# Optimization experiments

Hardware: AMD Instinct MI355X
Metric: run time of the kernel (lower is better)

The kernel has to match this reference:

```python
import jax, jax.numpy as jnp
import numpy as np

N = 2708       # hardcoded in the original forward (Cora)
INS = 1433
OUTS = 64
M = 8          # N_mechs
HID = 64       # conditioner hidden width
LEAK = 0.2
NEG = -1e9


def setup_inputs() -> dict:
    key = jax.random.key(0)
    ks = jax.random.split(key, 9)
    x = jax.random.normal(ks[0], (N, INS), dtype=jnp.float32)
    adj = jax.random.randint(ks[1], (N, N), 0, 2) > 0  # bool mask
    adj = adj | jnp.eye(N, dtype=bool)                 # ensure self-loops so softmax is well-defined
    s = 1.0 / np.sqrt(INS)
    W = jax.random.normal(ks[2], (M, INS, OUTS), dtype=jnp.float32) * s
    a_src = jax.random.normal(ks[3], (M, OUTS), dtype=jnp.float32) * (1.0 / np.sqrt(OUTS))
    a_dst = jax.random.normal(ks[4], (M, OUTS), dtype=jnp.float32) * (1.0 / np.sqrt(OUTS))
    Wc1 = jax.random.normal(ks[5], (INS, HID), dtype=jnp.float32) * s
    bc1 = jnp.zeros((HID,), dtype=jnp.float32)
    Wc2 = jax.random.normal(ks[6], (HID, 2 * M), dtype=jnp.float32) * (1.0 / np.sqrt(HID))
    bc2 = jnp.zeros((2 * M,), dtype=jnp.float32)
    return {"x": x, "adj": adj, "W": W, "a_src": a_src, "a_dst": a_dst,
            "Wc1": Wc1, "bc1": bc1, "Wc2": Wc2, "bc2": bc2}


def reference(x, adj, W, a_src, a_dst, Wc1, bc1, Wc2, bc2):
    # dropout is identity in eval mode.
    # Conditioner MLP applied per node (vectorized over the Python loop in the original):
    cond = jax.nn.relu(x @ Wc1 + bc1) @ Wc2 + bc2          # [N, 2M]
    c = cond.reshape(N, 2, M)                               # matches cond.view(2708, 2, -1)
    gamma = c[:, 0, :].T                                    # [M, N] per-node scalar gamma per mechanism
    beta = c[:, 1, :].T                                     # [M, N]
    # All mechanisms batched: project + FiLM modulate
    h = jnp.einsum('nf,mfo->mno', x, W)                     # [M, N, OUTS]
    h = gamma[:, :, None] * h + beta[:, :, None]
    # GAT scoring: e_ij = LeakyReLU(a_src.h_i + a_dst.h_j), masked by adj
    e_src = jnp.einsum('mno,mo->mn', h, a_src)              # [M, N]
    e_dst = jnp.einsum('mno,mo->mn', h, a_dst)              # [M, N]
    e = jax.nn.leaky_relu(e_src[:, :, None] + e_dst[:, None, :], LEAK)  # [M, N, N]
    e = jnp.where(adj[None, :, :], e, NEG)
    attn = jax.nn.softmax(e, axis=-1)                       # [M, N, N]
    out = jnp.einsum('mnk,mko->mno', attn, h)               # [M, N, OUTS]
    # concat=True: cat over mechanisms along feature dim
    out = jnp.transpose(out, (1, 0, 2)).reshape(N, M * OUTS)  # [N, M*OUTS]
    return out
```

## Files before the change

kernel.cpp:

```cpp
#include <hip/hip_runtime.h>

#define NN   2708
#define INS  1433
#define MM   8
#define NP   2720
#define WPR  85
#define KP   1440
#define NKC  45
#define RP   2752
#define C9   576
#define OC   512

#define CAN_ASRC 0
#define CAN_ADST 512
#define CAN_BC1  1024
#define CAN_BC2  1088
#define CAN_WC2  1104
#define CAN_TOT  2128

#define XBLK 15480

typedef unsigned short u16;
typedef unsigned int   u32;
typedef __attribute__((ext_vector_type(8))) short bf16x8;
typedef __attribute__((ext_vector_type(4))) float f32x4;

static __device__ __forceinline__ u16 f2bfu(float f) {
    union { float f; u32 u; } v; v.f = f;
    u32 u = v.u;
    u32 r = (u + 0x7fffu + ((u >> 16) & 1u)) >> 16;
    return (u16)r;
}
static __device__ __forceinline__ float bfu2f(u16 b) {
    union { u32 u; float f; } v; v.u = ((u32)b) << 16;
    return v.f;
}

static __device__ __forceinline__ int xfp32_of(const int* ctr) { return ctr[0] > 32; }
static __device__ __forceinline__ int aflag_of(const int* ctr) {
    if (ctr[2]) return 3;
    if (ctr[3]) return 4;
    if (ctr[4]) return 5;
    if (ctr[1]) return 1;
    if (ctr[5]) return 0;
    return 2;
}

__global__ void k_init(int* ctr) { if (threadIdx.x < 8) ctr[threadIdx.x] = 0; }

__global__ void k_probe_x(const u32* __restrict__ x_raw, int* __restrict__ ctr) {
    int local = 0;
    for (int w = blockIdx.x * 256 + threadIdx.x; w < 65536; w += 32 * 256) {
        u32 v = x_raw[w];
        u32 lo = v & 0xffffu, hi = v >> 16;
        if ((lo & 0x7f80u) == 0u && lo != 0u) local++;
        if ((hi & 0x7f80u) == 0u && hi != 0u) local++;
    }
    #pragma unroll
    for (int off = 32; off > 0; off >>= 1) local += __shfl_xor(local, off, 64);
    if ((threadIdx.x & 63) == 0 && local) atomicAdd(&ctr[0], local);
}

__global__ void k_probe_adj(const u32* __restrict__ adj_raw, int* __restrict__ ctr) {
    int f_gt1 = 0, f_bf16 = 0, f_f32 = 0, f_f16 = 0, f_odd = 0;
    for (int w = blockIdx.x * 256 + threadIdx.x; w < 65536; w += 32 * 256) {
        u32 v = adj_raw[w];
        f_bf16 |= (v == 0x3f803f80u);
        f_f32  |= (v == 0x3f800000u);
        f_f16  |= (v == 0x3c003c00u);
        f_gt1  |= (v > 1u);
        f_odd  |= ((w & 1) && v != 0u);
    }
    int a1 = __any(f_gt1), a2 = __any(f_bf16), a3 = __any(f_f32),
        a4 = __any(f_f16), a5 = __any(f_odd);
    if ((threadIdx.x & 63) == 0) {
        if (a1) atomicOr(&ctr[1], 1);
        if (a2) atomicOr(&ctr[2], 1);
        if (a3) atomicOr(&ctr[3], 1);
        if (a4) atomicOr(&ctr[4], 1);
        if (a5) atomicOr(&ctr[5], 1);
    }
}

static __device__ __forceinline__ u16 load_as_bf16(const void* p, size_t idx, int fp32) {
    if (fp32) return f2bfu(((const float*)p)[idx]);
    return ((const u16*)p)[idx];
}
static __device__ __forceinline__ float load_as_f32(const void* p, size_t idx, int fp32) {
    if (fp32) return ((const float*)p)[idx];
    return bfu2f(((const u16*)p)[idx]);
}

__global__ void k_pack_x(const void* __restrict__ x, const void* a_src, const void* a_dst,
                         const void* bc1, const void* bc2, const void* Wc2,
                         u16* __restrict__ xpf, float* __restrict__ canon,
                         const int* __restrict__ ctr) {
    const int fp32 = xfp32_of(ctr);
    const int bid = blockIdx.x;
    if (bid < XBLK) {
        int e = bid * 256 + threadIdx.x;
        int t1 = e >> 9, sub = e & 511;
        int r = sub >> 5, kloc = sub & 31;
        int it = t1 / NKC, kc = t1 - it * NKC;
        int row = it * 16 + r, col = kc * 32 + kloc;
        u16 v = 0;
        if (row < NN && col < INS) v = load_as_bf16(x, (size_t)row * INS + col, fp32);
        xpf[e] = v;
    } else {
        for (int e = threadIdx.x; e < CAN_TOT; e += 256) {
            float v;
            if      (e < CAN_ADST) v = load_as_f32(a_src, e - CAN_ASRC, fp32);
            else if (e < CAN_BC1)  v = load_as_f32(a_dst, e - CAN_ADST, fp32);
            else if (e < CAN_BC2)  v = load_as_f32(bc1,  e - CAN_BC1, fp32);
            else if (e < CAN_WC2)  v = load_as_f32(bc2,  e - CAN_BC2, fp32);
            else                   v = load_as_f32(Wc2,  e - CAN_WC2, fp32);
            canon[e] = v;
        }
    }
}

__global__ void k_pack_wt(const void* __restrict__ W, const void* __restrict__ Wc1,
                          u16* __restrict__ WTf, const int* __restrict__ ctr) {
    const int fp32 = xfp32_of(ctr);
    const int mblk = blockIdx.x, ktile = blockIdx.y;
    __shared__ float lds[64][65];
    #pragma unroll
    for (int ii = 0; ii < 16; ++ii) {
        int l = threadIdx.x * 16 + ii;
        int k_in = l >> 6, o = l & 63;
        int k = ktile * 64 + k_in;
        float v = 0.f;
        if (k < INS) {
            if (mblk < 8) v = load_as_f32(W, ((size_t)mblk * INS + k) * 64 + o, fp32);
            else          v = load_as_f32(Wc1, (size_t)k * 64 + o, fp32);
        }
        lds[k_in][o] = v;
    }
    __syncthreads();
    #pragma unroll
    for (int ii = 0; ii < 16; ++ii) {
        int e2 = threadIdx.x * 16 + ii;
        int ct2 = e2 >> 10, kc2 = (e2 >> 9) & 1;
        int r = (e2 >> 5) & 15, kloc = e2 & 31;
        int kc = ktile * 2 + kc2;
        if (kc < NKC) {
            int ct = mblk * 4 + ct2;
            WTf[(((size_t)ct * NKC + kc) * 16 + r) * 32 + kloc] =
                f2bfu(lds[kc2 * 32 + kloc][ct2 * 16 + r]);
        }
    }
}

#define WAVES_PER_ROW 43
__global__ void k_pack_adj(const void* __restrict__ adj, u32* __restrict__ adjT,
                           const int* __restrict__ ctr) {
    const int f = aflag_of(ctr);
    const int wid  = (blockIdx.x * 256 + threadIdx.x) >> 6;
    const int lane = threadIdx.x & 63;
    const int i  = wid / WAVES_PER_ROW;
    const int jb = (wid - i * WAVES_PER_ROW) * 64;
    if (i >= NN) return;
    const int j = jb + lane;
    int v = 0;
    if (j < NN) {
        size_t s = (size_t)i * NN + j;
        if      (f == 0) v = ((const int*)adj)[s] != 0;
        else if (f == 1) v = ((const unsigned char*)adj)[s] != 0;
        else if (f == 2) v = ((const long long*)adj)[s] != 0;
        else if (f == 4) v = ((const float*)adj)[s] != 0.f;
        else             v = ((const u16*)adj)[s] != 0;
    }
    unsigned long long mask = __ballot(v);
    if (lane == 0) {
        const int ww = jb >> 5;
        adjT[(size_t)ww * NP + i] = (u32)mask;
        if (ww + 1 < WPR) adjT[(size_t)(ww + 1) * NP + i] = (u32)(mask >> 32);
    }
}

__launch_bounds__(256)
__global__ void k_gemm(const u16* __restrict__ xpf, const u16* __restrict__ WTf,
                       float* __restrict__ h_pre) {
    const int wave = threadIdx.x >> 6;
    const int lane = threadIdx.x & 63;
    const int r    = lane & 15;
    const int quad = lane >> 4;
    const int it   = blockIdx.x * 4 + wave;
    const int ct0  = blockIdx.y * 4;

    const u16* aP = xpf + (size_t)it * NKC * 512 + r * 32 + quad * 8;
    const u16* bP = WTf + (size_t)ct0 * NKC * 512 + r * 32 + quad * 8;

    f32x4 acc[4];
    #pragma unroll
    for (int nt = 0; nt < 4; ++nt) acc[nt] = (f32x4){0.f, 0.f, 0.f, 0.f};

    #pragma unroll 3
    for (int kc = 0; kc < NKC; ++kc) {
        bf16x8 af = *(const bf16x8*)(aP + kc * 512);
        bf16x8 b0 = *(const bf16x8*)(bP + kc * 512);
        bf16x8 b1 = *(const bf16x8*)(bP + (size_t)NKC * 512 + kc * 512);
        bf16x8 b2 = *(const bf16x8*)(bP + (size_t)2 * NKC * 512 + kc * 512);
        bf16x8 b3 = *(const bf16x8*)(bP + (size_t)3 * NKC * 512 + kc * 512);
        acc[0] = __builtin_amdgcn_mfma_f32_16x16x32_bf16(af, b0, acc[0], 0, 0, 0);
        acc[1] = __builtin_amdgcn_mfma_f32_16x16x32_bf16(af, b1, acc[1], 0, 0, 0);
        acc[2] = __builtin_amdgcn_mfma_f32_16x16x32_bf16(af, b2, acc[2], 0, 0, 0);
        acc[3] = __builtin_amdgcn_mfma_f32_16x16x32_bf16(af, b3, acc[3], 0, 0, 0);
    }

    const int i_base = it * 16;
    const int c_base = blockIdx.y * 64;
    #pragma unroll
    for (int reg = 0; reg < 4; ++reg) {
        const int ii = i_base + quad * 4 + reg;
        if (ii < NN) {
            float* orow = h_pre + (size_t)ii * C9 + c_base;
            orow[ 0 + r] = acc[0][reg];
            orow[16 + r] = acc[1][reg];
            orow[32 + r] = acc[2][reg];
            orow[48 + r] = acc[3][reg];
        }
    }
}

__launch_bounds__(256)
__global__ void k_film(const float* __restrict__ h_pre, const float* __restrict__ canon,
                       u16* __restrict__ HTf, float* __restrict__ e_srcP,
                       float* __restrict__ e_dstP) {
    const int m  = blockIdx.y;
    const int t  = threadIdx.x;
    const int nl = t & 63;
    const int og = t >> 6;
    const int n  = blockIdx.x * 64 + nl;
    const bool valid   = n < NN;
    const bool inrange = n < NP;

    __shared__ float sh_a[4][64], sh_b[4][64];

    float pg = 0.f, pbv = 0.f;
    #pragma unroll
    for (int oo = 0; oo < 16; ++oo) {
        const int o = og * 16 + oo;
        float hv = 0.f;
        if (valid) hv = h_pre[(size_t)n * C9 + 512 + o] + canon[CAN_BC1 + o];
        hv = hv > 0.f ? hv : 0.f;
        pg  += hv * canon[CAN_WC2 + o * 16 + m];
        pbv += hv * canon[CAN_WC2 + o * 16 + m + 8];
    }
    sh_a[og][nl] = pg; sh_b[og][nl] = pbv;
    __syncthreads();
    const float g = sh_a[0][nl] + sh_a[1][nl] + sh_a[2][nl] + sh_a[3][nl] + canon[CAN_BC2 + m];
    const float b = sh_b[0][nl] + sh_b[1][nl] + sh_b[2][nl] + sh_b[3][nl] + canon[CAN_BC2 + m + 8];
    __syncthreads();

    const size_t hbase = ((size_t)m * WPR + (n >> 5)) * 2048 + (n & 31);
    float ps = 0.f, pd = 0.f;
    #pragma unroll
    for (int oo = 0; oo < 16; ++oo) {
        const int o = og * 16 + oo;
        float h = 0.f;
        if (valid) {
            h = g * h_pre[(size_t)n * C9 + m * 64 + o] + b;
            ps += h * canon[CAN_ASRC + m * 64 + o];
            pd += h * canon[CAN_ADST + m * 64 + o];
        }
        if (inrange) HTf[hbase + o * 32] = f2bfu(h);
    }
    sh_a[og][nl] = ps; sh_b[og][nl] = pd;
    __syncthreads();
    if (og == 0 && inrange) {
        e_srcP[m * NP + n] = sh_a[0][nl] + sh_a[1][nl] + sh_a[2][nl] + sh_a[3][nl];
        e_dstP[m * NP + n] = sh_b[0][nl] + sh_b[1][nl] + sh_b[2][nl] + sh_b[3][nl];
    }
}

__global__ void k_prep(const float* __restrict__ e_srcP, const float* __restrict__ e_dstP,
                       float* __restrict__ E1P, float* __restrict__ E2P,
                       float* __restrict__ F1P, float* __restrict__ F2P) {
    const int m = blockIdx.x, t = threadIdx.x;
    const float* ed = e_dstP + m * NP;
    const float* es = e_srcP + m * NP;
    float mx = -3.0e38f;
    for (int j = t; j < NP; j += 256) mx = fmaxf(mx, ed[j]);
    #pragma unroll
    for (int off = 32; off > 0; off >>= 1) mx = fmaxf(mx, __shfl_xor(mx, off, 64));
    __shared__ float sm[4];
    if ((t & 63) == 0) sm[t >> 6] = mx;
    __syncthreads();
    const float maxd = fmaxf(fmaxf(sm[0], sm[1]), fmaxf(sm[2], sm[3]));
    for (int j = t; j < NP; j += 256) {
        const float d = ed[j] - maxd;
        E1P[m * NP + j] = __expf(d);
        E2P[m * NP + j] = __expf(0.2f * d);
    }
    for (int i = t; i < NP; i += 256) {
        const float v = es[i] + maxd;
        const float rmax = v > 0.f ? v : 0.2f * v;
        F1P[m * NP + i] = __expf(v - rmax);
        F2P[m * NP + i] = __expf(0.2f * v - rmax);
    }
}

__launch_bounds__(256)
__global__ void k_attn(const u32* __restrict__ adjT, const float* __restrict__ F1P,
                       const float* __restrict__ F2P, const float* __restrict__ E1P,
                       const float* __restrict__ E2P, const u16* __restrict__ HTf,
                       void* __restrict__ outv, const int* __restrict__ ctr) {
    const int m    = blockIdx.y;
    const int i0   = blockIdx.x * 16;
    const int wave = threadIdx.x >> 6;
    const int lane = threadIdx.x & 63;
    const int r    = lane & 15;
    const int quad = lane >> 4;
    const int i    = (i0 + r < NN) ? (i0 + r) : (NN - 1);

    const float F1 = F1P[m * NP + i];
    const float F2 = F2P[m * NP + i];
    const float* e1row = E1P + m * NP;
    const float* e2row = E2P + m * NP;
    const u16* hbase = HTf + (size_t)m * WPR * 2048 + r * 32 + quad * 8;

    f32x4 acc[4], accl;
    #pragma unroll
    for (int nt = 0; nt < 4; ++nt) acc[nt] = (f32x4){0.f, 0.f, 0.f, 0.f};
    accl = (f32x4){0.f, 0.f, 0.f, 0.f};

    bf16x8 ones;
    #pragma unroll
    for (int kk = 0; kk < 8; ++kk) ones[kk] = (short)0x3f80;

    #pragma unroll 2
    for (int jc = wave * 32; jc < NP; jc += 128) {
        const int jb = jc + quad * 8;
        const int tile = jc >> 5;
        const float4 a0 = *(const float4*)(e1row + jb);
        const float4 a1 = *(const float4*)(e1row + jb + 4);
        const float4 b0 = *(const float4*)(e2row + jb);
        const float4 b1 = *(const float4*)(e2row + jb + 4);
        const u32 w = adjT[(size_t)tile * NP + i];
        const u32 mask8 = (w >> (quad * 8)) & 0xffu;
        float p[8];
        p[0] = fmaxf(F1 * a0.x, F2 * b0.x);
        p[1] = fmaxf(F1 * a0.y, F2 * b0.y);
        p[2] = fmaxf(F1 * a0.z, F2 * b0.z);
        p[3] = fmaxf(F1 * a0.w, F2 * b0.w);
        p[4] = fmaxf(F1 * a1.x, F2 * b1.x);
        p[5] = fmaxf(F1 * a1.y, F2 * b1.y);
        p[6] = fmaxf(F1 * a1.z, F2 * b1.z);
        p[7] = fmaxf(F1 * a1.w, F2 * b1.w);
        bf16x8 af;
        #pragma unroll
        for (int kk = 0; kk < 8; ++kk) {
            const float pv = ((mask8 >> kk) & 1u) ? p[kk] : 0.f;
            af[kk] = (short)f2bfu(pv);
        }
        const u16* ht = hbase + (size_t)tile * 2048;
        #pragma unroll
        for (int nt = 0; nt < 4; ++nt) {
            bf16x8 bf = *(const bf16x8*)(ht + nt * 512);
            acc[nt] = __builtin_amdgcn_mfma_f32_16x16x32_bf16(af, bf, acc[nt], 0, 0, 0);
        }
        accl = __builtin_amdgcn_mfma_f32_16x16x32_bf16(af, ones, accl, 0, 0, 0);
    }

    __shared__ float red[4][64][21];
    #pragma unroll
    for (int nt = 0; nt < 4; ++nt)
        #pragma unroll
        for (int reg = 0; reg < 4; ++reg)
            red[wave][lane][nt * 4 + reg] = acc[nt][reg];
    #pragma unroll
    for (int reg = 0; reg < 4; ++reg)
        red[wave][lane][16 + reg] = accl[reg];
    __syncthreads();
    if (wave != 0) return;

    #pragma unroll
    for (int nt = 0; nt < 4; ++nt)
        #pragma unroll
        for (int reg = 0; reg < 4; ++reg)
            acc[nt][reg] = red[0][lane][nt * 4 + reg] + red[1][lane][nt * 4 + reg]
                         + red[2][lane][nt * 4 + reg] + red[3][lane][nt * 4 + reg];
    #pragma unroll
    for (int reg = 0; reg < 4; ++reg)
        accl[reg] = red[0][lane][16 + reg] + red[1][lane][16 + reg]
                  + red[2][lane][16 + reg] + red[3][lane][16 + reg];

    const int ofp32 = xfp32_of(ctr);
    #pragma unroll
    for (int reg = 0; reg < 4; ++reg) {
        const int ii = i0 + quad * 4 + reg;
        if (ii < NN) {
            const float lr = accl[reg];
            const float inv = (lr > 0.f) ? 1.f / lr : 0.f;
            #pragma unroll
            for (int nt = 0; nt < 4; ++nt) {
                const float o = acc[nt][reg] * inv;
                const size_t idx = (size_t)ii * OC + m * 64 + nt * 16 + r;
                if (ofp32) ((float*)outv)[idx] = o;
                else       ((u16*)outv)[idx]   = f2bfu(o);
            }
        }
    }
}

extern "C" void kernel_launch(void* const* d_in, const int* in_sizes, int n_in,
                              void* d_out, int out_size, void* d_ws, size_t ws_size,
                              hipStream_t stream) {
    (void)in_sizes; (void)n_in; (void)out_size; (void)ws_size;
    const void* x     = d_in[0];
    const void* adj   = d_in[1];
    const void* W     = d_in[2];
    const void* a_src = d_in[3];
    const void* a_dst = d_in[4];
    const void* Wc1   = d_in[5];
    const void* bc1   = d_in[6];
    const void* Wc2   = d_in[7];
    const void* bc2   = d_in[8];

    char* ws = (char*)d_ws;
    size_t off = 0;
    auto alloc = [&](size_t bytes) -> void* {
        void* p = ws + off;
        off += (bytes + 255) & ~(size_t)255;
        return p;
    };
    u16*   xpf     = (u16*)  alloc((size_t)RP * KP * 2);
    u16*   WTf     = (u16*)  alloc((size_t)C9 * KP * 2);
    float* h_pre   = (float*)alloc((size_t)NN * C9 * 4);
    float* e_srcP  = (float*)alloc((size_t)MM * NP * 4);
    float* e_dstP  = (float*)alloc((size_t)MM * NP * 4);
    float* E1P     = (float*)alloc((size_t)MM * NP * 4);
    float* E2P     = (float*)alloc((size_t)MM * NP * 4);
    float* F1P     = (float*)alloc((size_t)MM * NP * 4);
    float* F2P     = (float*)alloc((size_t)MM * NP * 4);
    u16*   HTf     = (u16*)  alloc((size_t)MM * WPR * 2048 * 2);
    u32*   adjT    = (u32*)  alloc((size_t)WPR * NP * 4);
    float* canon   = (float*)alloc((size_t)CAN_TOT * 4);
    int*   ctr     = (int*)  alloc(256);

    hipLaunchKernelGGL(k_init, dim3(1), dim3(64), 0, stream, ctr);
    hipLaunchKernelGGL(k_probe_x, dim3(32), dim3(256), 0, stream, (const u32*)x, ctr);
    hipLaunchKernelGGL(k_probe_adj, dim3(32), dim3(256), 0, stream, (const u32*)adj, ctr);
    hipLaunchKernelGGL(k_pack_x, dim3(XBLK + 1), dim3(256), 0, stream,
                       x, a_src, a_dst, bc1, bc2, Wc2, xpf, canon, ctr);
    hipLaunchKernelGGL(k_pack_wt, dim3(9, 23), dim3(256), 0, stream, W, Wc1, WTf, ctr);
    {
        const int waves = NN * WAVES_PER_ROW;
        hipLaunchKernelGGL(k_pack_adj, dim3((waves + 3) / 4), dim3(256), 0, stream, adj, adjT, ctr);
    }
    hipLaunchKernelGGL(k_gemm, dim3(RP / 64, 9), dim3(256), 0, stream, xpf, WTf, h_pre);
    hipLaunchKernelGGL(k_film, dim3((NP + 63) / 64, MM), dim3(256), 0, stream,
                       h_pre, canon, HTf, e_srcP, e_dstP);
    hipLaunchKernelGGL(k_prep, dim3(MM), dim3(256), 0, stream,
                       e_srcP, e_dstP, E1P, E2P, F1P, F2P);
    hipLaunchKernelGGL(k_attn, dim3((NN + 15) / 16, MM), dim3(256), 0, stream,
                       adjT, F1P, F2P, E1P, E2P, HTf, d_out, ctr);
}
```

Measured before the change: 232.7 us.

## Fuse probe and pack kernels, reshape gemm blocks, restructure film and attention tiling

Merges the two probe kernels and the init kernel into one probe that writes per-block partials, so no zeroing pass or atomics are needed. The three pack kernels (adj, x, weights) become a single launch. The gemm switches to single-wave blocks. FiLM now uses wave-shuffle reductions with an LDS transpose for coalesced HTf writes. Attention handles 32 rows per block so each loaded H tile feeds two MFMA row sets. Together these cut launch overhead and reload traffic, at the cost of more registers and LDS in the attention kernel and every thread re-reading 32 counters to decode the flags.

```diff
diff --git a/kernel.cpp b/kernel.cpp
--- a/kernel.cpp
+++ b/kernel.cpp
@@ -18,7 +18,11 @@
 #define CAN_WC2  1104
 #define CAN_TOT  2128
 
-#define XBLK 15480
+#define ADJ_WAVES (NN * 43)
+#define ADJBLK ((ADJ_WAVES + 3) / 4)
+#define XBLK   15480
+#define WTBLK  (9 * 23)
+#define PACK_TOT (ADJBLK + XBLK + WTBLK + 1)
 
 typedef unsigned short u16;
 typedef unsigned int   u32;
@@ -36,49 +40,59 @@
     return v.f;
 }
 
-static __device__ __forceinline__ int xfp32_of(const int* ctr) { return ctr[0] > 32; }
+static __device__ __forceinline__ int xfp32_of(const int* ctr) {
+    int s = 0;
+    #pragma unroll
+    for (int k = 0; k < 32; ++k) s += ctr[k];
+    return s > 32;
+}
 static __device__ __forceinline__ int aflag_of(const int* ctr) {
-    if (ctr[2]) return 3;
-    if (ctr[3]) return 4;
-    if (ctr[4]) return 5;
-    if (ctr[1]) return 1;
-    if (ctr[5]) return 0;
+    int b = 0;
+    #pragma unroll
+    for (int k = 32; k < 64; ++k) b |= ctr[k];
+    if (b & 2)  return 3;
+    if (b & 4)  return 4;
+    if (b & 8)  return 5;
+    if (b & 1)  return 1;
+    if (b & 16) return 0;
     return 2;
 }
 
-__global__ void k_init(int* ctr) { if (threadIdx.x < 8) ctr[threadIdx.x] = 0; }
-
-__global__ void k_probe_x(const u32* __restrict__ x_raw, int* __restrict__ ctr) {
-    int local = 0;
-    for (int w = blockIdx.x * 256 + threadIdx.x; w < 65536; w += 32 * 256) {
-        u32 v = x_raw[w];
-        u32 lo = v & 0xffffu, hi = v >> 16;
-        if ((lo & 0x7f80u) == 0u && lo != 0u) local++;
-        if ((hi & 0x7f80u) == 0u && hi != 0u) local++;
-    }
-    #pragma unroll
-    for (int off = 32; off > 0; off >>= 1) local += __shfl_xor(local, off, 64);
-    if ((threadIdx.x & 63) == 0 && local) atomicAdd(&ctr[0], local);
-}
-
-__global__ void k_probe_adj(const u32* __restrict__ adj_raw, int* __restrict__ ctr) {
-    int f_gt1 = 0, f_bf16 = 0, f_f32 = 0, f_f16 = 0, f_odd = 0;
-    for (int w = blockIdx.x * 256 + threadIdx.x; w < 65536; w += 32 * 256) {
-        u32 v = adj_raw[w];
-        f_bf16 |= (v == 0x3f803f80u);
-        f_f32  |= (v == 0x3f800000u);
-        f_f16  |= (v == 0x3c003c00u);
-        f_gt1  |= (v > 1u);
-        f_odd  |= ((w & 1) && v != 0u);
-    }
-    int a1 = __any(f_gt1), a2 = __any(f_bf16), a3 = __any(f_f32),
-        a4 = __any(f_f16), a5 = __any(f_odd);
-    if ((threadIdx.x & 63) == 0) {
-        if (a1) atomicOr(&ctr[1], 1);
-        if (a2) atomicOr(&ctr[2], 1);
-        if (a3) atomicOr(&ctr[3], 1);
-        if (a4) atomicOr(&ctr[4], 1);
-        if (a5) atomicOr(&ctr[5], 1);
+__global__ void k_probe(const u32* __restrict__ x_raw, const u32* __restrict__ adj_raw,
+                        int* __restrict__ ctr) {
+    const int b = blockIdx.x, t = threadIdx.x;
+    __shared__ int sred[4];
+    if (b < 32) {
+        int local = 0;
+        #pragma unroll
+        for (int k = 0; k < 8; ++k) {
+            u32 v = x_raw[b * 2048 + k * 256 + t];
+            u32 lo = v & 0xffffu, hi = v >> 16;
+            if ((lo & 0x7f80u) == 0u && lo != 0u) local++;
+            if ((hi & 0x7f80u) == 0u && hi != 0u) local++;
+        }
+        #pragma unroll
+        for (int off = 32; off > 0; off >>= 1) local += __shfl_xor(local, off, 64);
+        if ((t & 63) == 0) sred[t >> 6] = local;
+        __syncthreads();
+        if (t == 0) ctr[b] = sred[0] + sred[1] + sred[2] + sred[3];
+    } else {
+        int fl = 0;
+        #pragma unroll
+        for (int k = 0; k < 8; ++k) {
+            int w = (b - 32) * 2048 + k * 256 + t;
+            u32 v = adj_raw[w];
+            if (v > 1u)           fl |= 1;
+            if (v == 0x3f803f80u) fl |= 2;
+            if (v == 0x3f800000u) fl |= 4;
+            if (v == 0x3c003c00u) fl |= 8;
+            if ((w & 1) && v)     fl |= 16;
+        }
+        #pragma unroll
+        for (int off = 32; off > 0; off >>= 1) fl |= __shfl_xor(fl, off, 64);
+        if ((t & 63) == 0) sred[t >> 6] = fl;
+        __syncthreads();
+        if (t == 0) ctr[b] = sred[0] | sred[1] | sred[2] | sred[3];
     }
 }
 
@@ -91,14 +105,41 @@
     return bfu2f(((const u16*)p)[idx]);
 }
 
-__global__ void k_pack_x(const void* __restrict__ x, const void* a_src, const void* a_dst,
-                         const void* bc1, const void* bc2, const void* Wc2,
-                         u16* __restrict__ xpf, float* __restrict__ canon,
-                         const int* __restrict__ ctr) {
-    const int fp32 = xfp32_of(ctr);
+__global__ void k_pack(const void* __restrict__ x, const void* __restrict__ adj,
+                       const void* __restrict__ W, const void* __restrict__ Wc1,
+                       const void* a_src, const void* a_dst, const void* bc1,
+                       const void* bc2, const void* Wc2,
+                       u16* __restrict__ xpf, u16* __restrict__ WTf,
+                       u32* __restrict__ adjT, float* __restrict__ canon,
+                       const int* __restrict__ ctr) {
+    __shared__ float lds[64][65];
     const int bid = blockIdx.x;
-    if (bid < XBLK) {
-        int e = bid * 256 + threadIdx.x;
+    if (bid < ADJBLK) {
+        const int f = aflag_of(ctr);
+        const int wid  = bid * 4 + (threadIdx.x >> 6);
+        const int lane = threadIdx.x & 63;
+        const int i  = wid / 43;
+        const int jb = (wid - i * 43) * 64;
+        if (i >= NN) return;
+        const int j = jb + lane;
+        int v = 0;
+        if (j < NN) {
+            size_t s = (size_t)i * NN + j;
+            if      (f == 0) v = ((const int*)adj)[s] != 0;
+            else if (f == 1) v = ((const unsigned char*)adj)[s] != 0;
+            else if (f == 2) v = ((const long long*)adj)[s] != 0;
+            else if (f == 4) v = ((const float*)adj)[s] != 0.f;
+            else             v = ((const u16*)adj)[s] != 0;
+        }
+        unsigned long long mask = __ballot(v);
+        if (lane == 0) {
+            const int ww = jb >> 5;
+            adjT[(size_t)ww * NP + i] = (u32)mask;
+            if (ww + 1 < WPR) adjT[(size_t)(ww + 1) * NP + i] = (u32)(mask >> 32);
+        }
+    } else if (bid < ADJBLK + XBLK) {
+        const int fp32 = xfp32_of(ctr);
+        int e = (bid - ADJBLK) * 256 + threadIdx.x;
         int t1 = e >> 9, sub = e & 511;
         int r = sub >> 5, kloc = sub & 31;
         int it = t1 / NKC, kc = t1 - it * NKC;
@@ -106,7 +147,37 @@
         u16 v = 0;
         if (row < NN && col < INS) v = load_as_bf16(x, (size_t)row * INS + col, fp32);
         xpf[e] = v;
+    } else if (bid < ADJBLK + XBLK + WTBLK) {
+        const int fp32 = xfp32_of(ctr);
+        const int b2 = bid - ADJBLK - XBLK;
+        const int mblk = b2 / 23, ktile = b2 - mblk * 23;
+        #pragma unroll
+        for (int ii = 0; ii < 16; ++ii) {
+            int l = threadIdx.x * 16 + ii;
+            int k_in = l >> 6, o = l & 63;
+            int k = ktile * 64 + k_in;
+            float v = 0.f;
+            if (k < INS) {
+                if (mblk < 8) v = load_as_f32(W, ((size_t)mblk * INS + k) * 64 + o, fp32);
+                else          v = load_as_f32(Wc1, (size_t)k * 64 + o, fp32);
+            }
+            lds[k_in][o] = v;
+        }
+        __syncthreads();
+        #pragma unroll
+        for (int ii = 0; ii < 16; ++ii) {
+            int e2 = threadIdx.x * 16 + ii;
+            int ct2 = e2 >> 10, kc2 = (e2 >> 9) & 1;
+            int r = (e2 >> 5) & 15, kloc = e2 & 31;
+            int kc = ktile * 2 + kc2;
+            if (kc < NKC) {
+                int ct = mblk * 4 + ct2;
+                WTf[(((size_t)ct * NKC + kc) * 16 + r) * 32 + kloc] =
+                    f2bfu(lds[kc2 * 32 + kloc][ct2 * 16 + r]);
+            }
+        }
     } else {
+        const int fp32 = xfp32_of(ctr);
         for (int e = threadIdx.x; e < CAN_TOT; e += 256) {
             float v;
             if      (e < CAN_ADST) v = load_as_f32(a_src, e - CAN_ASRC, fp32);
@@ -119,73 +190,13 @@
     }
 }
 
-__global__ void k_pack_wt(const void* __restrict__ W, const void* __restrict__ Wc1,
-                          u16* __restrict__ WTf, const int* __restrict__ ctr) {
-    const int fp32 = xfp32_of(ctr);
-    const int mblk = blockIdx.x, ktile = blockIdx.y;
-    __shared__ float lds[64][65];
-    #pragma unroll
-    for (int ii = 0; ii < 16; ++ii) {
-        int l = threadIdx.x * 16 + ii;
-        int k_in = l >> 6, o = l & 63;
-        int k = ktile * 64 + k_in;
-        float v = 0.f;
-        if (k < INS) {
-            if (mblk < 8) v = load_as_f32(W, ((size_t)mblk * INS + k) * 64 + o, fp32);
-            else          v = load_as_f32(Wc1, (size_t)k * 64 + o, fp32);
-        }
-        lds[k_in][o] = v;
-    }
-    __syncthreads();
-    #pragma unroll
-    for (int ii = 0; ii < 16; ++ii) {
-        int e2 = threadIdx.x * 16 + ii;
-        int ct2 = e2 >> 10, kc2 = (e2 >> 9) & 1;
-        int r = (e2 >> 5) & 15, kloc = e2 & 31;
-        int kc = ktile * 2 + kc2;
-        if (kc < NKC) {
-            int ct = mblk * 4 + ct2;
-            WTf[(((size_t)ct * NKC + kc) * 16 + r) * 32 + kloc] =
-                f2bfu(lds[kc2 * 32 + kloc][ct2 * 16 + r]);
-        }
-    }
-}
-
-#define WAVES_PER_ROW 43
-__global__ void k_pack_adj(const void* __restrict__ adj, u32* __restrict__ adjT,
-                           const int* __restrict__ ctr) {
-    const int f = aflag_of(ctr);
-    const int wid  = (blockIdx.x * 256 + threadIdx.x) >> 6;
-    const int lane = threadIdx.x & 63;
-    const int i  = wid / WAVES_PER_ROW;
-    const int jb = (wid - i * WAVES_PER_ROW) * 64;
-    if (i >= NN) return;
-    const int j = jb + lane;
-    int v = 0;
-    if (j < NN) {
-        size_t s = (size_t)i * NN + j;
-        if      (f == 0) v = ((const int*)adj)[s] != 0;
-        else if (f == 1) v = ((const unsigned char*)adj)[s] != 0;
-        else if (f == 2) v = ((const long long*)adj)[s] != 0;
-        else if (f == 4) v = ((const float*)adj)[s] != 0.f;
-        else             v = ((const u16*)adj)[s] != 0;
-    }
-    unsigned long long mask = __ballot(v);
-    if (lane == 0) {
-        const int ww = jb >> 5;
-        adjT[(size_t)ww * NP + i] = (u32)mask;
-        if (ww + 1 < WPR) adjT[(size_t)(ww + 1) * NP + i] = (u32)(mask >> 32);
-    }
-}
-
-__launch_bounds__(256)
+__launch_bounds__(64)
 __global__ void k_gemm(const u16* __restrict__ xpf, const u16* __restrict__ WTf,
                        float* __restrict__ h_pre) {
-    const int wave = threadIdx.x >> 6;
-    const int lane = threadIdx.x & 63;
+    const int lane = threadIdx.x;
     const int r    = lane & 15;
     const int quad = lane >> 4;
-    const int it   = blockIdx.x * 4 + wave;
+    const int it   = blockIdx.x;
     const int ct0  = blockIdx.y * 4;
 
     const u16* aP = xpf + (size_t)it * NKC * 512 + r * 32 + quad * 8;
@@ -228,49 +239,49 @@
                        u16* __restrict__ HTf, float* __restrict__ e_srcP,
                        float* __restrict__ e_dstP) {
     const int m  = blockIdx.y;
-    const int t  = threadIdx.x;
-    const int nl = t & 63;
-    const int og = t >> 6;
-    const int n  = blockIdx.x * 64 + nl;
-    const bool valid   = n < NN;
-    const bool inrange = n < NP;
-
-    __shared__ float sh_a[4][64], sh_b[4][64];
-
-    float pg = 0.f, pbv = 0.f;
-    #pragma unroll
-    for (int oo = 0; oo < 16; ++oo) {
-        const int o = og * 16 + oo;
+    const int n0 = blockIdx.x * 32;
+    const int t  = threadIdx.x, wave = t >> 6, o = t & 63;
+    __shared__ u16 hbuf[32][66];
+
+    const float wg = canon[CAN_WC2 + o * 16 + m];
+    const float wb = canon[CAN_WC2 + o * 16 + m + 8];
+    const float as = canon[CAN_ASRC + m * 64 + o];
+    const float ad = canon[CAN_ADST + m * 64 + o];
+    const float b1 = canon[CAN_BC1 + o];
+    const float g0 = canon[CAN_BC2 + m], b0 = canon[CAN_BC2 + m + 8];
+
+    #pragma unroll
+    for (int it = 0; it < 8; ++it) {
+        const int nl = wave * 8 + it, n = n0 + nl;
+        const bool valid = n < NN;
         float hv = 0.f;
-        if (valid) hv = h_pre[(size_t)n * C9 + 512 + o] + canon[CAN_BC1 + o];
+        if (valid) hv = h_pre[(size_t)n * C9 + 512 + o] + b1;
         hv = hv > 0.f ? hv : 0.f;
-        pg  += hv * canon[CAN_WC2 + o * 16 + m];
-        pbv += hv * canon[CAN_WC2 + o * 16 + m + 8];
-    }
-    sh_a[og][nl] = pg; sh_b[og][nl] = pbv;
+        float pg = hv * wg, pb = hv * wb;
+        #pragma unroll
+        for (int off = 32; off > 0; off >>= 1) {
+            pg += __shfl_xor(pg, off, 64);
+            pb += __shfl_xor(pb, off, 64);
+        }
+        const float g = pg + g0, bb = pb + b0;
+        float h = 0.f;
+        if (valid) h = g * h_pre[(size_t)n * C9 + m * 64 + o] + bb;
+        float ps = h * as, pd = h * ad;
+        #pragma unroll
+        for (int off = 32; off > 0; off >>= 1) {
+            ps += __shfl_xor(ps, off, 64);
+            pd += __shfl_xor(pd, off, 64);
+        }
+        if (o == 0) { e_srcP[m * NP + n] = ps; e_dstP[m * NP + n] = pd; }
+        hbuf[nl][o] = f2bfu(h);
+    }
     __syncthreads();
-    const float g = sh_a[0][nl] + sh_a[1][nl] + sh_a[2][nl] + sh_a[3][nl] + canon[CAN_BC2 + m];
-    const float b = sh_b[0][nl] + sh_b[1][nl] + sh_b[2][nl] + sh_b[3][nl] + canon[CAN_BC2 + m + 8];
-    __syncthreads();
-
-    const size_t hbase = ((size_t)m * WPR + (n >> 5)) * 2048 + (n & 31);
-    float ps = 0.f, pd = 0.f;
-    #pragma unroll
-    for (int oo = 0; oo < 16; ++oo) {
-        const int o = og * 16 + oo;
-        float h = 0.f;
-        if (valid) {
-            h = g * h_pre[(size_t)n * C9 + m * 64 + o] + b;
-            ps += h * canon[CAN_ASRC + m * 64 + o];
-            pd += h * canon[CAN_ADST + m * 64 + o];
-        }
-        if (inrange) HTf[hbase + o * 32] = f2bfu(h);
-    }
-    sh_a[og][nl] = ps; sh_b[og][nl] = pd;
-    __syncthreads();
-    if (og == 0 && inrange) {
-        e_srcP[m * NP + n] = sh_a[0][nl] + sh_a[1][nl] + sh_a[2][nl] + sh_a[3][nl];
-        e_dstP[m * NP + n] = sh_b[0][nl] + sh_b[1][nl] + sh_b[2][nl] + sh_b[3][nl];
+    u32* ht32 = (u32*)(HTf + ((size_t)m * WPR + (n0 >> 5)) * 2048);
+    #pragma unroll
+    for (int rep = 0; rep < 4; ++rep) {
+        const int idx = rep * 256 + t;
+        const int oo = idx >> 4, jp = idx & 15;
+        ht32[idx] = (u32)hbuf[2 * jp][oo] | ((u32)hbuf[2 * jp + 1][oo] << 16);
     }
 }
 
@@ -306,30 +317,31 @@
                        const float* __restrict__ F2P, const float* __restrict__ E1P,
                        const float* __restrict__ E2P, const u16* __restrict__ HTf,
                        void* __restrict__ outv, const int* __restrict__ ctr) {
-    const int m    = blockIdx.y;
-    const int i0   = blockIdx.x * 16;
-    const int wave = threadIdx.x >> 6;
-    const int lane = threadIdx.x & 63;
-    const int r    = lane & 15;
-    const int quad = lane >> 4;
-    const int i    = (i0 + r < NN) ? (i0 + r) : (NN - 1);
-
-    const float F1 = F1P[m * NP + i];
-    const float F2 = F2P[m * NP + i];
+    const int m = blockIdx.y, i0 = blockIdx.x * 32;
+    const int wave = threadIdx.x >> 6, lane = threadIdx.x & 63;
+    const int r = lane & 15, quad = lane >> 4;
+    const int iA = min(i0 + r, NN - 1);
+    const int iB = min(i0 + 16 + r, NN - 1);
+
+    const float F1a = F1P[m * NP + iA], F2a = F2P[m * NP + iA];
+    const float F1b = F1P[m * NP + iB], F2b = F2P[m * NP + iB];
     const float* e1row = E1P + m * NP;
     const float* e2row = E2P + m * NP;
     const u16* hbase = HTf + (size_t)m * WPR * 2048 + r * 32 + quad * 8;
 
-    f32x4 acc[4], accl;
-    #pragma unroll
-    for (int nt = 0; nt < 4; ++nt) acc[nt] = (f32x4){0.f, 0.f, 0.f, 0.f};
-    accl = (f32x4){0.f, 0.f, 0.f, 0.f};
+    f32x4 accA[4], accB[4], lA, lB;
+    #pragma unroll
+    for (int nt = 0; nt < 4; ++nt) {
+        accA[nt] = (f32x4){0.f, 0.f, 0.f, 0.f};
+        accB[nt] = (f32x4){0.f, 0.f, 0.f, 0.f};
+    }
+    lA = (f32x4){0.f, 0.f, 0.f, 0.f};
+    lB = (f32x4){0.f, 0.f, 0.f, 0.f};
 
     bf16x8 ones;
     #pragma unroll
     for (int kk = 0; kk < 8; ++kk) ones[kk] = (short)0x3f80;
 
-    #pragma unroll 2
     for (int jc = wave * 32; jc < NP; jc += 128) {
         const int jb = jc + quad * 8;
         const int tile = jc >> 5;
@@ -337,68 +349,80 @@
         const float4 a1 = *(const float4*)(e1row + jb + 4);
         const float4 b0 = *(const float4*)(e2row + jb);
         const float4 b1 = *(const float4*)(e2row + jb + 4);
-        const u32 w = adjT[(size_t)tile * NP + i];
-        const u32 mask8 = (w >> (quad * 8)) & 0xffu;
-        float p[8];
-        p[0] = fmaxf(F1 * a0.x, F2 * b0.x);
-        p[1] = fmaxf(F1 * a0.y, F2 * b0.y);
-        p[2] = fmaxf(F1 * a0.z, F2 * b0.z);
-        p[3] = fmaxf(F1 * a0.w, F2 * b0.w);
-        p[4] = fmaxf(F1 * a1.x, F2 * b1.x);
-        p[5] = fmaxf(F1 * a1.y, F2 * b1.y);
-        p[6] = fmaxf(F1 * a1.z, F2 * b1.z);
-        p[7] = fmaxf(F1 * a1.w, F2 * b1.w);
-        bf16x8 af;
+        const u32 wA = adjT[(size_t)tile * NP + iA];
+        const u32 wB = adjT[(size_t)tile * NP + iB];
+        const u32 mA = (wA >> (quad * 8)) & 0xffu;
+        const u32 mB = (wB >> (quad * 8)) & 0xffu;
+        float e1[8] = {a0.x, a0.y, a0.z, a0.w, a1.x, a1.y, a1.z, a1.w};
+        float e2[8] = {b0.x, b0.y, b0.z, b0.w, b1.x, b1.y, b1.z, b1.w};
+        bf16x8 afA, afB;
         #pragma unroll
         for (int kk = 0; kk < 8; ++kk) {
-            const float pv = ((mask8 >> kk) & 1u) ? p[kk] : 0.f;
-            af[kk] = (short)f2bfu(pv);
+            float pa = fmaxf(F1a * e1[kk], F2a * e2[kk]);
+            float pb = fmaxf(F1b * e1[kk], F2b * e2[kk]);
+            afA[kk] = (short)f2bfu(((mA >> kk) & 1u) ? pa : 0.f);
+            afB[kk] = (short)f2bfu(((mB >> kk) & 1u) ? pb : 0.f);
         }
         const u16* ht = hbase + (size_t)tile * 2048;
         #pragma unroll
         for (int nt = 0; nt < 4; ++nt) {
             bf16x8 bf = *(const bf16x8*)(ht + nt * 512);
-            acc[nt] = __builtin_amdgcn_mfma_f32_16x16x32_bf16(af, bf, acc[nt], 0, 0, 0);
-        }
-        accl = __builtin_amdgcn_mfma_f32_16x16x32_bf16(af, ones, accl, 0, 0, 0);
-    }
-
-    __shared__ float red[4][64][21];
+            accA[nt] = __builtin_amdgcn_mfma_f32_16x16x32_bf16(afA, bf, accA[nt], 0, 0, 0);
+            accB[nt] = __builtin_amdgcn_mfma_f32_16x16x32_bf16(afB, bf, accB[nt], 0, 0, 0);
+        }
+        lA = __builtin_amdgcn_mfma_f32_16x16x32_bf16(afA, ones, lA, 0, 0, 0);
+        lB = __builtin_amdgcn_mfma_f32_16x16x32_bf16(afB, ones, lB, 0, 0, 0);
+    }
+
+    __shared__ float red[4][64][42];
     #pragma unroll
     for (int nt = 0; nt < 4; ++nt)
         #pragma unroll
-        for (int reg = 0; reg < 4; ++reg)
-            red[wave][lane][nt * 4 + reg] = acc[nt][reg];
-    #pragma unroll
-    for (int reg = 0; reg < 4; ++reg)
-        red[wave][lane][16 + reg] = accl[reg];
+        for (int reg = 0; reg < 4; ++reg) {
+            red[wave][lane][nt * 4 + reg]      = accA[nt][reg];
+            red[wave][lane][16 + nt * 4 + reg] = accB[nt][reg];
+        }
+    #pragma unroll
+    for (int reg = 0; reg < 4; ++reg) {
+        red[wave][lane][32 + reg] = lA[reg];
+        red[wave][lane][36 + reg] = lB[reg];
+    }
     __syncthreads();
     if (wave != 0) return;
 
     #pragma unroll
     for (int nt = 0; nt < 4; ++nt)
         #pragma unroll
-        for (int reg = 0; reg < 4; ++reg)
-            acc[nt][reg] = red[0][lane][nt * 4 + reg] + red[1][lane][nt * 4 + reg]
-                         + red[2][lane][nt * 4 + reg] + red[3][lane][nt * 4 + reg];
-    #pragma unroll
-    for (int reg = 0; reg < 4; ++reg)
-        accl[reg] = red[0][lane][16 + reg] + red[1][lane][16 + reg]
-                  + red[2][lane][16 + reg] + red[3][lane][16 + reg];
+        for (int reg = 0; reg < 4; ++reg) {
+            accA[nt][reg] = red[0][lane][nt * 4 + reg] + red[1][lane][nt * 4 + reg]
+                          + red[2][lane][nt * 4 + reg] + red[3][lane][nt * 4 + reg];
+            accB[nt][reg] = red[0][lane][16 + nt * 4 + reg] + red[1][lane][16 + nt * 4 + reg]
+                          + red[2][lane][16 + nt * 4 + reg] + red[3][lane][16 + nt * 4 + reg];
+        }
+    #pragma unroll
+    for (int reg = 0; reg < 4; ++reg) {
+        lA[reg] = red[0][lane][32 + reg] + red[1][lane][32 + reg]
+                + red[2][lane][32 + reg] + red[3][lane][32 + reg];
+        lB[reg] = red[0][lane][36 + reg] + red[1][lane][36 + reg]
+                + red[2][lane][36 + reg] + red[3][lane][36 + reg];
+    }
 
     const int ofp32 = xfp32_of(ctr);
     #pragma unroll
-    for (int reg = 0; reg < 4; ++reg) {
-        const int ii = i0 + quad * 4 + reg;
-        if (ii < NN) {
-            const float lr = accl[reg];
-            const float inv = (lr > 0.f) ? 1.f / lr : 0.f;
-            #pragma unroll
-            for (int nt = 0; nt < 4; ++nt) {
-                const float o = acc[nt][reg] * inv;
-                const size_t idx = (size_t)ii * OC + m * 64 + nt * 16 + r;
-                if (ofp32) ((float*)outv)[idx] = o;
-                else       ((u16*)outv)[idx]   = f2bfu(o);
+    for (int s = 0; s < 2; ++s) {
+        #pragma unroll
+        for (int reg = 0; reg < 4; ++reg) {
+            const int ii = i0 + s * 16 + quad * 4 + reg;
+            if (ii < NN) {
+                const float lr = s ? lB[reg] : lA[reg];
+                const float inv = (lr > 0.f) ? 1.f / lr : 0.f;
+                #pragma unroll
+                for (int nt = 0; nt < 4; ++nt) {
+                    const float o = (s ? accB[nt][reg] : accA[nt][reg]) * inv;
+                    const size_t idx = (size_t)ii * OC + m * 64 + nt * 16 + r;
+                    if (ofp32) ((float*)outv)[idx] = o;
+                    else       ((u16*)outv)[idx]   = f2bfu(o);
+                }
             }
         }
     }
@@ -439,21 +463,16 @@
     float* canon   = (float*)alloc((size_t)CAN_TOT * 4);
     int*   ctr     = (int*)  alloc(256);
 
-    hipLaunchKernelGGL(k_init, dim3(1), dim3(64), 0, stream, ctr);
-    hipLaunchKernelGGL(k_probe_x, dim3(32), dim3(256), 0, stream, (const u32*)x, ctr);
-    hipLaunchKernelGGL(k_probe_adj, dim3(32), dim3(256), 0, stream, (const u32*)adj, ctr);
-    hipLaunchKernelGGL(k_pack_x, dim3(XBLK + 1), dim3(256), 0, stream,
-                       x, a_src, a_dst, bc1, bc2, Wc2, xpf, canon, ctr);
-    hipLaunchKernelGGL(k_pack_wt, dim3(9, 23), dim3(256), 0, stream, W, Wc1, WTf, ctr);
-    {
-        const int waves = NN * WAVES_PER_ROW;
-        hipLaunchKernelGGL(k_pack_adj, dim3((waves + 3) / 4), dim3(256), 0, stream, adj, adjT, ctr);
-    }
-    hipLaunchKernelGGL(k_gemm, dim3(RP / 64, 9), dim3(256), 0, stream, xpf, WTf, h_pre);
-    hipLaunchKernelGGL(k_film, dim3((NP + 63) / 64, MM), dim3(256), 0, stream,
+    hipLaunchKernelGGL(k_probe, dim3(64), dim3(256), 0, stream,
+                       (const u32*)x, (const u32*)adj, ctr);
+    hipLaunchKernelGGL(k_pack, dim3(PACK_TOT), dim3(256), 0, stream,
+                       x, adj, W, Wc1, a_src, a_dst, bc1, bc2, Wc2,
+                       xpf, WTf, adjT, canon, ctr);
+    hipLaunchKernelGGL(k_gemm, dim3(RP / 16, 9), dim3(64), 0, stream, xpf, WTf, h_pre);
+    hipLaunchKernelGGL(k_film, dim3(NP / 32, MM), dim3(256), 0, stream,
                        h_pre, canon, HTf, e_srcP, e_dstP);
     hipLaunchKernelGGL(k_prep, dim3(MM), dim3(256), 0, stream,
                        e_srcP, e_dstP, E1P, E2P, F1P, F2P);
-    hipLaunchKernelGGL(k_attn, dim3((NN + 15) / 16, MM), dim3(256), 0, stream,
+    hipLaunchKernelGGL(k_attn, dim3(NP / 32, MM), dim3(256), 0, stream,
                        adjT, F1P, F2P, E1P, E2P, HTf, d_out, ctr);
 }
```

Result: slower. 254.3 us (+9.3%).
